# Performance work log

Measured on AMD Instinct MI355X. Metric: run time of the kernel, lower is better.

Reference implementation:

```python
import jax, jax.numpy as jnp
import numpy as np

L = 16          # n_levels
F = 2           # n_features_per_level
LOG2_T = 19
T = 1 << LOG2_T # hashmap size per level
BASE_RES = 16
FINEST_RES = 2048
_b = (FINEST_RES / BASE_RES) ** (1.0 / (L - 1))
RES = [int(np.floor(BASE_RES * _b ** l)) for l in range(L)]
PRIMES = (1, 2654435761, 805459861, 3674653429)
H = 2 * L * F   # 64 = n_neurons (static 32 + dynamic 32)
N_PTS = 2097152


def hash_encode(coords, table):
    """Multi-resolution hash grid encoding. coords [N,D] in [0,1], table [L,T,F] -> [N, L*F]."""
    N, D = coords.shape
    # 2^D corner offsets of the enclosing grid cell
    offsets = np.stack(
        np.meshgrid(*([np.array([0, 1], dtype=np.uint32)] * D), indexing='ij'), -1
    ).reshape(-1, D)
    primes = [jnp.uint32(p) for p in PRIMES[:D]]
    feats = []
    for l in range(L):  # fixed small loop over levels
        pos = coords * RES[l]
        grid = jnp.floor(pos)
        frac = pos - grid                       # [N,D] interpolation weights
        gu = grid.astype(jnp.int32).astype(jnp.uint32)
        acc = jnp.zeros((N, F), coords.dtype)
        for off in offsets:                     # fixed 2^D corners
            idx = gu + off[None, :]
            h = idx[:, 0] * primes[0]
            for d in range(1, D):
                h = h ^ (idx[:, d] * primes[d])
            h = (h & jnp.uint32(T - 1)).astype(jnp.int32)
            w = jnp.prod(jnp.where(off[None, :] != 0, frac, 1.0 - frac), axis=1)
            acc = acc + w[:, None] * table[l, h]
        feats.append(acc)
    return jnp.concatenate(feats, -1)


def setup_inputs() -> dict:
    key = jax.random.key(0)
    ks = jax.random.split(key, 12)
    s = 1.0 / np.sqrt(H)
    return {
        'x': jax.random.uniform(ks[0], (N_PTS, 3), jnp.float32),
        't': jax.random.uniform(ks[1], (), jnp.float32),
        'table_static': jax.random.uniform(ks[2], (L, T, F), jnp.float32, -1e-4, 1e-4),
        'table_dynamic': jax.random.uniform(ks[3], (L, T, F), jnp.float32, -1e-4, 1e-4),
        'w1_0': jax.random.normal(ks[4], (H, H), jnp.float32) * s,
        'w1_1': jax.random.normal(ks[5], (H, H), jnp.float32) * s,
        'w1_2': jax.random.normal(ks[6], (H, H), jnp.float32) * s,
        'w2_0': jax.random.normal(ks[7], (H, H), jnp.float32) * s,
        'w2_1': jax.random.normal(ks[8], (H, H), jnp.float32) * s,
        'w2_2': jax.random.normal(ks[9], (H, 1), jnp.float32) * s,
        'skip_alpha': jnp.float32(0.5),
    }


def reference(x, t, table_static, table_dynamic, w1_0, w1_1, w1_2,
              w2_0, w2_1, w2_2, skip_alpha):
    relu = jax.nn.relu
    # t_input = cat([x, full((N,1), t)])
    t_col = jnp.broadcast_to(t.astype(x.dtype), (x.shape[0], 1))
    t_input = jnp.concatenate([x, t_col], axis=1)
    static_features = hash_encode(x, table_static)          # [N,32]
    dynamic_features = hash_encode(t_input, table_dynamic)  # [N,32]
    feat = jnp.concatenate([static_features, dynamic_features], -1)  # [N,64]
    # net_1: 2 hidden layers, ReLU everywhere incl. output activation
    h = relu(feat @ w1_0)
    h = relu(h @ w1_1)
    out1 = relu(h @ w1_2)
    # adaptive skip blend
    blend = out1 * skip_alpha + (1.0 - skip_alpha) * feat
    # net_2: 2 hidden layers ReLU, linear output -> [N,1]
    h = relu(blend @ w2_0)
    h = relu(h @ w2_1)
    return h @ w2_2
```

## Files before the change

kernel.cpp:

```cpp
#include <hip/hip_runtime.h>
#include <math.h>

#define LVLS 16
#define TMASK ((1u << 19) - 1u)
#define NT 256
#define TSLICE (1u << 20)
#define KPL (1u << 19)

typedef _Float16 h4 __attribute__((ext_vector_type(4)));
typedef short bf8i __attribute__((ext_vector_type(8)));
typedef float f4 __attribute__((ext_vector_type(4)));

#define ESCALE 1024.0f
#define EINV   0.0009765625f

struct ResParams { float rf[LVLS]; };

__device__ __forceinline__ unsigned hash3(unsigned ux, unsigned uy, unsigned uz) {
    return ux ^ (uy * 2654435761u) ^ (uz * 805459861u);
}

__device__ __forceinline__ unsigned short bf16_rne(float f) {
    unsigned u = __builtin_bit_cast(unsigned, f);
    unsigned r = (u + 0x7FFFu + ((u >> 16) & 1u)) >> 16;
    return (unsigned short)r;
}
__device__ __forceinline__ float bf16_to_f(unsigned short h) {
    unsigned u = ((unsigned)h) << 16;
    return __builtin_bit_cast(float, u);
}
__device__ __forceinline__ void split8(const float* v, bf8i& h, bf8i& l) {
    #pragma unroll
    for (int j = 0; j < 8; ++j) {
        unsigned short hb = bf16_rne(v[j]);
        h[j] = (short)hb;
        l[j] = (short)bf16_rne(v[j] - bf16_to_f(hb));
    }
}

__global__ __launch_bounds__(NT, 8)
void build_E(const float* __restrict__ tabs, const float* __restrict__ tabd,
             const float* __restrict__ t_ptr, h4* __restrict__ E, ResParams rp)
{
    const unsigned idx = blockIdx.x * NT + threadIdx.x;
    const unsigned l = idx >> 19;
    const unsigned k = idx & TMASK;
    const float r = rp.rf[l];
    const float tt = t_ptr[0];
    const float ft = tt * r;
    const float gt = floorf(ft);
    const float wt = ft - gt;
    const unsigned ut = (unsigned)(int)gt;
    const unsigned c0 = (ut * 3674653429u) & TMASK;
    const unsigned c1 = ((ut + 1u) * 3674653429u) & TMASK;
    const float* ts = tabs + (size_t)l * TSLICE;
    const float* td = tabd + (size_t)l * TSLICE;
    const float2 s  = *(const float2*)(ts + (size_t)k * 2u);
    const float2 d0 = *(const float2*)(td + (size_t)(k ^ c0) * 2u);
    const float2 d1 = *(const float2*)(td + (size_t)(k ^ c1) * 2u);
    const float om = 1.f - wt;
    h4 v;
    v.x = (_Float16)(s.x * ESCALE);
    v.y = (_Float16)(s.y * ESCALE);
    v.z = (_Float16)((om * d0.x + wt * d1.x) * ESCALE);
    v.w = (_Float16)((om * d0.y + wt * d1.y) * ESCALE);
    E[idx] = v;
}

__global__ __launch_bounds__(NT)
void build_W(const float* __restrict__ w10, const float* __restrict__ w11,
             const float* __restrict__ w12, const float* __restrict__ w20,
             const float* __restrict__ w21, const float* __restrict__ w22,
             unsigned short* __restrict__ Wf)
{
    const int tid = blockIdx.x * NT + threadIdx.x;
    if (tid >= 6 * 4 * 2 * 64) return;
    const int lane = tid & 63;
    const int ks = (tid >> 6) & 1;
    const int nt = (tid >> 7) & 3;
    const int L  = tid >> 9;
    const int g = lane >> 4, c = lane & 15;
    unsigned short* dst = Wf + (size_t)tid * 16;
    #pragma unroll
    for (int j = 0; j < 8; ++j) {
        const int k = ks * 32 + g * 8 + j;
        float v;
        if      (L == 0) v = w10[k * 64 + nt * 16 + c];
        else if (L == 1) v = w11[k * 64 + nt * 16 + c];
        else if (L == 2) v = w12[k * 64 + nt * 16 + c];
        else if (L == 3) v = w20[k * 64 + nt * 16 + c];
        else if (L == 4) v = w21[k * 64 + nt * 16 + c];
        else             v = (nt == 0 && c == 0) ? w22[k] : 0.f;
        unsigned short hb = bf16_rne(v);
        unsigned short lb = bf16_rne(v - bf16_to_f(hb));
        dst[j]     = hb;
        dst[8 + j] = lb;
    }
}

__global__ __launch_bounds__(NT, 8)
void enc_all(const float* __restrict__ x, const h4* __restrict__ E,
             float2* __restrict__ fb, long cp, int npts, ResParams rp)
{
    const int l = blockIdx.y;
    const int gid = blockIdx.x * NT + threadIdx.x;
    if (gid >= npts) return;
    const float r = rp.rf[l];
    const h4* Es = E + (size_t)l * KPL;
    float2* fbs = fb + (size_t)l * cp;
    float2* fbd = fb + (size_t)(LVLS + l) * cp;

    const float px = x[3 * gid + 0];
    const float py = x[3 * gid + 1];
    const float pz = x[3 * gid + 2];
    const float fx = px * r, fy = py * r, fz = pz * r;
    const float gx = floorf(fx), gy = floorf(fy), gz = floorf(fz);
    const float wx = fx - gx, wy = fy - gy, wz = fz - gz;
    const unsigned ux = (unsigned)(int)gx;
    const unsigned uy = (unsigned)(int)gy;
    const unsigned uz = (unsigned)(int)gz;
    float a0 = 0.f, a1 = 0.f, b0 = 0.f, b1 = 0.f;
    #pragma unroll
    for (int cc = 0; cc < 8; ++cc) {
        const unsigned ox = (cc >> 2) & 1, oy = (cc >> 1) & 1, oz = cc & 1;
        const unsigned kk = hash3(ux + ox, uy + oy, uz + oz) & TMASK;
        const float w = (ox ? wx : 1.f - wx)
                      * (oy ? wy : 1.f - wy)
                      * (oz ? wz : 1.f - wz);
        const h4 e = Es[kk];
        a0 = fmaf(w, (float)e.x, a0);
        a1 = fmaf(w, (float)e.y, a1);
        b0 = fmaf(w, (float)e.z, b0);
        b1 = fmaf(w, (float)e.w, b1);
    }
    fbs[gid] = make_float2(a0 * EINV, a1 * EINV);
    fbd[gid] = make_float2(b0 * EINV, b1 * EINV);
}

#define MLPT 128
__global__ __launch_bounds__(MLPT)
void mlp_mfma(const float2* __restrict__ fb, long cp, const uint4* __restrict__ Wf,
              const float* __restrict__ alpha_ptr, float* __restrict__ out, int npts)
{
    __shared__ float XBs[2][64 * 68];
    const int lane = threadIdx.x & 63;
    const int wv   = threadIdx.x >> 6;
    const int base = blockIdx.x * MLPT + wv * 64;
    if (base >= npts) return;
    float* xb = XBs[wv];
    const int g = lane >> 4, c = lane & 15;
    const float alpha = alpha_ptr[0];
    const float oma = 1.f - alpha;

    bf8i ah[4][2], al[4][2];

    #pragma unroll
    for (int mt = 0; mt < 4; ++mt)
      #pragma unroll
      for (int ks = 0; ks < 2; ++ks) {
        float tmp[8];
        #pragma unroll
        for (int jj = 0; jj < 4; ++jj) {
            const float2 v = fb[(long)(ks * 16 + g * 4 + jj) * cp + base + mt * 16 + c];
            tmp[2 * jj] = v.x; tmp[2 * jj + 1] = v.y;
        }
        split8(tmp, ah[mt][ks], al[mt][ks]);
      }

    auto run_layer = [&](int Lidx, bool relu) {
        #pragma unroll
        for (int nt = 0; nt < 4; ++nt) {
            const uint4* wp0 = Wf + ((size_t)(((Lidx * 4 + nt) * 2 + 0) * 64 + lane)) * 2;
            const uint4* wp1 = Wf + ((size_t)(((Lidx * 4 + nt) * 2 + 1) * 64 + lane)) * 2;
            const bf8i wh0 = __builtin_bit_cast(bf8i, wp0[0]);
            const bf8i wl0 = __builtin_bit_cast(bf8i, wp0[1]);
            const bf8i wh1 = __builtin_bit_cast(bf8i, wp1[0]);
            const bf8i wl1 = __builtin_bit_cast(bf8i, wp1[1]);
            f4 acc[4];
            #pragma unroll
            for (int mt = 0; mt < 4; ++mt) acc[mt] = (f4){0.f, 0.f, 0.f, 0.f};
            #pragma unroll
            for (int mt = 0; mt < 4; ++mt)
                acc[mt] = __builtin_amdgcn_mfma_f32_16x16x32_bf16(ah[mt][0], wh0, acc[mt], 0, 0, 0);
            #pragma unroll
            for (int mt = 0; mt < 4; ++mt)
                acc[mt] = __builtin_amdgcn_mfma_f32_16x16x32_bf16(ah[mt][1], wh1, acc[mt], 0, 0, 0);
            #pragma unroll
            for (int mt = 0; mt < 4; ++mt)
                acc[mt] = __builtin_amdgcn_mfma_f32_16x16x32_bf16(ah[mt][0], wl0, acc[mt], 0, 0, 0);
            #pragma unroll
            for (int mt = 0; mt < 4; ++mt)
                acc[mt] = __builtin_amdgcn_mfma_f32_16x16x32_bf16(ah[mt][1], wl1, acc[mt], 0, 0, 0);
            #pragma unroll
            for (int mt = 0; mt < 4; ++mt)
                acc[mt] = __builtin_amdgcn_mfma_f32_16x16x32_bf16(al[mt][0], wh0, acc[mt], 0, 0, 0);
            #pragma unroll
            for (int mt = 0; mt < 4; ++mt)
                acc[mt] = __builtin_amdgcn_mfma_f32_16x16x32_bf16(al[mt][1], wh1, acc[mt], 0, 0, 0);
            #pragma unroll
            for (int mt = 0; mt < 4; ++mt)
              #pragma unroll
              for (int r = 0; r < 4; ++r) {
                float v = acc[mt][r];
                if (relu) v = fmaxf(v, 0.f);
                xb[(mt * 16 + g * 4 + r) * 68 + nt * 16 + c] = v;
              }
        }
    };

    auto load_frags = [&](bool blend) {
        asm volatile("s_waitcnt lgkmcnt(0)" ::: "memory");
        #pragma unroll
        for (int mt = 0; mt < 4; ++mt)
          #pragma unroll
          for (int ks = 0; ks < 2; ++ks) {
            const float* row = &xb[(mt * 16 + c) * 68 + ks * 32 + g * 8];
            float tmp[8];
            #pragma unroll
            for (int j = 0; j < 8; ++j) tmp[j] = row[j];
            if (blend) {
                #pragma unroll
                for (int jj = 0; jj < 4; ++jj) {
                    const float2 v = fb[(long)(ks * 16 + g * 4 + jj) * cp + base + mt * 16 + c];
                    tmp[2 * jj]     = fmaf(tmp[2 * jj],     alpha, oma * v.x);
                    tmp[2 * jj + 1] = fmaf(tmp[2 * jj + 1], alpha, oma * v.y);
                }
            }
            split8(tmp, ah[mt][ks], al[mt][ks]);
          }
        asm volatile("s_waitcnt lgkmcnt(0)" ::: "memory");
    };

    run_layer(0, true);
    load_frags(false);
    run_layer(1, true);
    load_frags(false);
    run_layer(2, true);
    load_frags(true);
    run_layer(3, true);
    load_frags(false);
    run_layer(4, true);
    load_frags(false);

    {
        const uint4* wp0 = Wf + ((size_t)(((5 * 4 + 0) * 2 + 0) * 64 + lane)) * 2;
        const uint4* wp1 = Wf + ((size_t)(((5 * 4 + 0) * 2 + 1) * 64 + lane)) * 2;
        const bf8i wh0 = __builtin_bit_cast(bf8i, wp0[0]);
        const bf8i wl0 = __builtin_bit_cast(bf8i, wp0[1]);
        const bf8i wh1 = __builtin_bit_cast(bf8i, wp1[0]);
        const bf8i wl1 = __builtin_bit_cast(bf8i, wp1[1]);
        f4 acc[4];
        #pragma unroll
        for (int mt = 0; mt < 4; ++mt) acc[mt] = (f4){0.f, 0.f, 0.f, 0.f};
        #pragma unroll
        for (int mt = 0; mt < 4; ++mt)
            acc[mt] = __builtin_amdgcn_mfma_f32_16x16x32_bf16(ah[mt][0], wh0, acc[mt], 0, 0, 0);
        #pragma unroll
        for (int mt = 0; mt < 4; ++mt)
            acc[mt] = __builtin_amdgcn_mfma_f32_16x16x32_bf16(ah[mt][1], wh1, acc[mt], 0, 0, 0);
        #pragma unroll
        for (int mt = 0; mt < 4; ++mt)
            acc[mt] = __builtin_amdgcn_mfma_f32_16x16x32_bf16(ah[mt][0], wl0, acc[mt], 0, 0, 0);
        #pragma unroll
        for (int mt = 0; mt < 4; ++mt)
            acc[mt] = __builtin_amdgcn_mfma_f32_16x16x32_bf16(ah[mt][1], wl1, acc[mt], 0, 0, 0);
        #pragma unroll
        for (int mt = 0; mt < 4; ++mt)
            acc[mt] = __builtin_amdgcn_mfma_f32_16x16x32_bf16(al[mt][0], wh0, acc[mt], 0, 0, 0);
        #pragma unroll
        for (int mt = 0; mt < 4; ++mt)
            acc[mt] = __builtin_amdgcn_mfma_f32_16x16x32_bf16(al[mt][1], wh1, acc[mt], 0, 0, 0);
        if (c == 0) {
            #pragma unroll
            for (int mt = 0; mt < 4; ++mt) {
                float4 st = make_float4(acc[mt][0], acc[mt][1], acc[mt][2], acc[mt][3]);
                *reinterpret_cast<float4*>(&out[base + mt * 16 + g * 4]) = st;
            }
        }
    }
}

__global__ __launch_bounds__(NT, 2)
void hashmlp_fused(const float* __restrict__ x, const float* __restrict__ t_ptr,
                   const float* __restrict__ tab_s, const float* __restrict__ tab_d,
                   const float* __restrict__ w10, const float* __restrict__ w11,
                   const float* __restrict__ w12, const float* __restrict__ w20,
                   const float* __restrict__ w21, const float* __restrict__ w22,
                   const float* __restrict__ alpha_ptr, float* __restrict__ out,
                   int n, ResParams rp)
{
    __shared__ float smem[64 * NT];
    const int tid = threadIdx.x;
    const int gid = blockIdx.x * NT + tid;
    if (gid >= n) return;
    const float px = x[3 * gid], py = x[3 * gid + 1], pz = x[3 * gid + 2];
    const float tt = t_ptr[0];
    const float alpha = alpha_ptr[0];
    float feat[64];
    #pragma unroll
    for (int l = 0; l < LVLS; ++l) {
        const float r = rp.rf[l];
        const float fx = px * r, fy = py * r, fz = pz * r;
        const float gx = floorf(fx), gy = floorf(fy), gz = floorf(fz);
        const float wx = fx - gx, wy = fy - gy, wz = fz - gz;
        const unsigned ux = (unsigned)(int)gx, uy = (unsigned)(int)gy, uz = (unsigned)(int)gz;
        const float* tb = tab_s + ((size_t)l << 20);
        float a0 = 0.f, a1 = 0.f;
        #pragma unroll
        for (int cc = 0; cc < 8; ++cc) {
            const unsigned ox = (cc >> 2) & 1, oy = (cc >> 1) & 1, oz = cc & 1;
            const unsigned idx = hash3(ux + ox, uy + oy, uz + oz) & TMASK;
            const float w = (ox ? wx : 1.f - wx) * (oy ? wy : 1.f - wy) * (oz ? wz : 1.f - wz);
            const float2 f = *reinterpret_cast<const float2*>(tb + ((size_t)idx * 2u));
            a0 = fmaf(w, f.x, a0); a1 = fmaf(w, f.y, a1);
        }
        feat[2 * l] = a0; feat[2 * l + 1] = a1;
    }
    #pragma unroll
    for (int l = 0; l < LVLS; ++l) {
        const float r = rp.rf[l];
        const float fx = px * r, fy = py * r, fz = pz * r;
        const float gx = floorf(fx), gy = floorf(fy), gz = floorf(fz);
        const float wx = fx - gx, wy = fy - gy, wz = fz - gz;
        const unsigned ux = (unsigned)(int)gx, uy = (unsigned)(int)gy, uz = (unsigned)(int)gz;
        const float ftp = tt * r;
        const float gt = floorf(ftp);
        const float wtp = ftp - gt;
        const unsigned ut = (unsigned)(int)gt;
        const unsigned ht0 = ut * 3674653429u;
        const unsigned ht1 = (ut + 1u) * 3674653429u;
        const float* tb = tab_d + ((size_t)l << 20);
        float a0 = 0.f, a1 = 0.f;
        #pragma unroll
        for (int cc = 0; cc < 8; ++cc) {
            const unsigned ox = (cc >> 2) & 1, oy = (cc >> 1) & 1, oz = cc & 1;
            const unsigned hs = hash3(ux + ox, uy + oy, uz + oz);
            const float ws = (ox ? wx : 1.f - wx) * (oy ? wy : 1.f - wy) * (oz ? wz : 1.f - wz);
            {
                const unsigned idx = (hs ^ ht0) & TMASK;
                const float w = ws * (1.f - wtp);
                const float2 f = *reinterpret_cast<const float2*>(tb + ((size_t)idx * 2u));
                a0 = fmaf(w, f.x, a0); a1 = fmaf(w, f.y, a1);
            }
            {
                const unsigned idx = (hs ^ ht1) & TMASK;
                const float w = ws * wtp;
                const float2 f = *reinterpret_cast<const float2*>(tb + ((size_t)idx * 2u));
                a0 = fmaf(w, f.x, a0); a1 = fmaf(w, f.y, a1);
            }
        }
        feat[32 + 2 * l] = a0; feat[33 + 2 * l] = a1;
    }
    #pragma unroll
    for (int i = 0; i < 64; ++i) smem[i * NT + tid] = feat[i];
    float acc[64];
    auto layer = [&](const float* __restrict__ W, bool do_relu) {
        #pragma unroll
        for (int j = 0; j < 64; ++j) acc[j] = 0.f;
        for (int i = 0; i < 64; ++i) {
            const float fi = smem[i * NT + tid];
            const float* wr = W + i * 64;
            #pragma unroll
            for (int j = 0; j < 64; ++j) acc[j] = fmaf(fi, wr[j], acc[j]);
        }
        #pragma unroll
        for (int j = 0; j < 64; ++j) {
            const float v = do_relu ? fmaxf(acc[j], 0.f) : acc[j];
            smem[j * NT + tid] = v;
        }
    };
    layer(w10, true); layer(w11, true); layer(w12, true);
    #pragma unroll
    for (int j = 0; j < 64; ++j) {
        const float o1 = smem[j * NT + tid];
        smem[j * NT + tid] = fmaf(o1, alpha, (1.f - alpha) * feat[j]);
    }
    layer(w20, true); layer(w21, true);
    float o = 0.f;
    for (int i = 0; i < 64; ++i) o = fmaf(smem[i * NT + tid], w22[i], o);
    out[gid] = o;
}

extern "C" void kernel_launch(void* const* d_in, const int* in_sizes, int n_in,
                              void* d_out, int out_size, void* d_ws, size_t ws_size,
                              hipStream_t stream) {
    (void)n_in; (void)out_size;
    const float* x     = (const float*)d_in[0];
    const float* t     = (const float*)d_in[1];
    const float* tabs  = (const float*)d_in[2];
    const float* tabd  = (const float*)d_in[3];
    const float* w10   = (const float*)d_in[4];
    const float* w11   = (const float*)d_in[5];
    const float* w12   = (const float*)d_in[6];
    const float* w20   = (const float*)d_in[7];
    const float* w21   = (const float*)d_in[8];
    const float* w22   = (const float*)d_in[9];
    const float* alpha = (const float*)d_in[10];
    float* out = (float*)d_out;
    const int n = in_sizes[0] / 3;

    ResParams rp;
    const double b = pow(2048.0 / 16.0, 1.0 / 15.0);
    for (int l = 0; l < LVLS; ++l)
        rp.rf[l] = (float)(int)floor(16.0 * pow(b, (double)l));

    const size_t E_BYTES = (size_t)LVLS * KPL * 8u;
    const size_t W_BYTES = 128u * 1024u;
    if (ws_size < E_BYTES + W_BYTES + 256u * 1024u) {
        dim3 grid((n + NT - 1) / NT), block(NT);
        hipLaunchKernelGGL(hashmlp_fused, grid, block, 0, stream,
                           x, t, tabs, tabd, w10, w11, w12, w20, w21, w22,
                           alpha, out, n, rp);
        return;
    }

    h4* E = (h4*)d_ws;
    unsigned short* Wf = (unsigned short*)((char*)d_ws + E_BYTES);
    float2* fb = (float2*)((char*)d_ws + E_BYTES + W_BYTES);
    long cp_cap = (long)((ws_size - E_BYTES - W_BYTES) / 256u) & ~255L;
    long cp = cp_cap < (long)n ? cp_cap : (long)n;

    {
        const unsigned total = LVLS * KPL;
        hipLaunchKernelGGL(build_E, dim3(total / NT), dim3(NT), 0, stream,
                           tabs, tabd, t, E, rp);
        hipLaunchKernelGGL(build_W, dim3(12), dim3(NT), 0, stream,
                           w10, w11, w12, w20, w21, w22, Wf);
    }

    for (long start = 0; start < n; start += cp) {
        const long m = (n - start) < cp ? (n - start) : cp;
        dim3 egrid((unsigned)((m + NT - 1) / NT), LVLS);
        hipLaunchKernelGGL(enc_all, egrid, dim3(NT), 0, stream,
                           x + 3 * start, E, fb, cp, (int)m, rp);
        dim3 mgrid((unsigned)((m + MLPT - 1) / MLPT));
        hipLaunchKernelGGL(mlp_mfma, mgrid, dim3(MLPT), 0, stream,
                           fb, cp, (const uint4*)Wf, alpha, out + start, (int)m);
    }
}
```

Before: 1.522 ms.

## Store intermediate features as packed fp16 scaled values with nontemporal stores

```diff
diff --git a/kernel.cpp b/kernel.cpp
--- a/kernel.cpp
+++ b/kernel.cpp
@@ -100,15 +100,13 @@
 
 __global__ __launch_bounds__(NT, 8)
 void enc_all(const float* __restrict__ x, const h4* __restrict__ E,
-             float2* __restrict__ fb, long cp, int npts, ResParams rp)
+             h4* __restrict__ fb, long cp, int npts, ResParams rp)
 {
     const int l = blockIdx.y;
     const int gid = blockIdx.x * NT + threadIdx.x;
     if (gid >= npts) return;
     const float r = rp.rf[l];
     const h4* Es = E + (size_t)l * KPL;
-    float2* fbs = fb + (size_t)l * cp;
-    float2* fbd = fb + (size_t)(LVLS + l) * cp;
 
     const float px = x[3 * gid + 0];
     const float py = x[3 * gid + 1];
@@ -133,13 +131,18 @@
         b0 = fmaf(w, (float)e.z, b0);
         b1 = fmaf(w, (float)e.w, b1);
     }
-    fbs[gid] = make_float2(a0 * EINV, a1 * EINV);
-    fbd[gid] = make_float2(b0 * EINV, b1 * EINV);
+    h4 v;
+    v.x = (_Float16)a0;
+    v.y = (_Float16)a1;
+    v.z = (_Float16)b0;
+    v.w = (_Float16)b1;
+    __builtin_nontemporal_store(__builtin_bit_cast(unsigned long long, v),
+                                (unsigned long long*)&fb[(size_t)l * cp + gid]);
 }
 
 #define MLPT 128
 __global__ __launch_bounds__(MLPT)
-void mlp_mfma(const float2* __restrict__ fb, long cp, const uint4* __restrict__ Wf,
+void mlp_mfma(const h4* __restrict__ fb, long cp, const uint4* __restrict__ Wf,
               const float* __restrict__ alpha_ptr, float* __restrict__ out, int npts)
 {
     __shared__ float XBs[2][64 * 68];
@@ -155,17 +158,17 @@
     bf8i ah[4][2], al[4][2];
 
     #pragma unroll
-    for (int mt = 0; mt < 4; ++mt)
-      #pragma unroll
-      for (int ks = 0; ks < 2; ++ks) {
-        float tmp[8];
+    for (int mt = 0; mt < 4; ++mt) {
+        float t0[8], t1[8];
         #pragma unroll
         for (int jj = 0; jj < 4; ++jj) {
-            const float2 v = fb[(long)(ks * 16 + g * 4 + jj) * cp + base + mt * 16 + c];
-            tmp[2 * jj] = v.x; tmp[2 * jj + 1] = v.y;
-        }
-        split8(tmp, ah[mt][ks], al[mt][ks]);
-      }
+            const h4 e = fb[(size_t)(g * 4 + jj) * cp + base + mt * 16 + c];
+            t0[2 * jj] = (float)e.x; t0[2 * jj + 1] = (float)e.y;
+            t1[2 * jj] = (float)e.z; t1[2 * jj + 1] = (float)e.w;
+        }
+        split8(t0, ah[mt][0], al[mt][0]);
+        split8(t1, ah[mt][1], al[mt][1]);
+    }
 
     auto run_layer = [&](int Lidx, bool relu) {
         #pragma unroll
@@ -211,23 +214,25 @@
     auto load_frags = [&](bool blend) {
         asm volatile("s_waitcnt lgkmcnt(0)" ::: "memory");
         #pragma unroll
-        for (int mt = 0; mt < 4; ++mt)
-          #pragma unroll
-          for (int ks = 0; ks < 2; ++ks) {
-            const float* row = &xb[(mt * 16 + c) * 68 + ks * 32 + g * 8];
-            float tmp[8];
-            #pragma unroll
-            for (int j = 0; j < 8; ++j) tmp[j] = row[j];
+        for (int mt = 0; mt < 4; ++mt) {
+            float t0[8], t1[8];
+            #pragma unroll
+            for (int j = 0; j < 8; ++j) t0[j] = xb[(mt * 16 + c) * 68 + g * 8 + j];
+            #pragma unroll
+            for (int j = 0; j < 8; ++j) t1[j] = xb[(mt * 16 + c) * 68 + 32 + g * 8 + j];
             if (blend) {
                 #pragma unroll
                 for (int jj = 0; jj < 4; ++jj) {
-                    const float2 v = fb[(long)(ks * 16 + g * 4 + jj) * cp + base + mt * 16 + c];
-                    tmp[2 * jj]     = fmaf(tmp[2 * jj],     alpha, oma * v.x);
-                    tmp[2 * jj + 1] = fmaf(tmp[2 * jj + 1], alpha, oma * v.y);
+                    const h4 e = fb[(size_t)(g * 4 + jj) * cp + base + mt * 16 + c];
+                    t0[2 * jj]     = fmaf(t0[2 * jj],     alpha, oma * (float)e.x);
+                    t0[2 * jj + 1] = fmaf(t0[2 * jj + 1], alpha, oma * (float)e.y);
+                    t1[2 * jj]     = fmaf(t1[2 * jj],     alpha, oma * (float)e.z);
+                    t1[2 * jj + 1] = fmaf(t1[2 * jj + 1], alpha, oma * (float)e.w);
                 }
             }
-            split8(tmp, ah[mt][ks], al[mt][ks]);
-          }
+            split8(t0, ah[mt][0], al[mt][0]);
+            split8(t1, ah[mt][1], al[mt][1]);
+        }
         asm volatile("s_waitcnt lgkmcnt(0)" ::: "memory");
     };
 
@@ -273,7 +278,8 @@
         if (c == 0) {
             #pragma unroll
             for (int mt = 0; mt < 4; ++mt) {
-                float4 st = make_float4(acc[mt][0], acc[mt][1], acc[mt][2], acc[mt][3]);
+                float4 st = make_float4(acc[mt][0] * EINV, acc[mt][1] * EINV,
+                                        acc[mt][2] * EINV, acc[mt][3] * EINV);
                 *reinterpret_cast<float4*>(&out[base + mt * 16 + g * 4]) = st;
             }
         }
@@ -416,8 +422,8 @@
 
     h4* E = (h4*)d_ws;
     unsigned short* Wf = (unsigned short*)((char*)d_ws + E_BYTES);
-    float2* fb = (float2*)((char*)d_ws + E_BYTES + W_BYTES);
-    long cp_cap = (long)((ws_size - E_BYTES - W_BYTES) / 256u) & ~255L;
+    h4* fb = (h4*)((char*)d_ws + E_BYTES + W_BYTES);
+    long cp_cap = (long)((ws_size - E_BYTES - W_BYTES) / 128u) & ~255L;
     long cp = cp_cap < (long)n ? cp_cap : (long)n;
 
     {
```

Result: faster. 1.435 ms (-5.7%).
